# Kernel tuning notes

Measured on AMD Instinct MI355X. Metric: run time of the kernel, lower is better.

Reference implementation:

```python
import jax, jax.numpy as jnp
import numpy as np

N, H, D = 65536, 8, 32      # n_points, num_heads, dim_per_head (h_dim)
CD = 3                      # coords_dim
NW = 3                      # num_w_per_dist
BS = 128                    # block_size
NH = 2                      # n_hashes


def layer_norm(x, g, b, eps=1e-5):
    mu = x.mean(-1, keepdims=True)
    var = ((x - mu) ** 2).mean(-1, keepdims=True)
    return (x - mu) * jax.lax.rsqrt(var + eps) * g + b


def hept_attn(q, k, v, pe, Wrpe):
    """HEPT-style LSH-sorted block-diagonal attention with relative-position kernel.
    q,k,v: (N,H,D); pe: (N,CD); Wrpe: (NW*(CD-1), H*D) (w_rpe.weight^T).
    score_ij = q_i.k_j/sqrt(D) - sum_r omega[h,r]*(p_i,r - p_j,r)^2 within LSH blocks.
    """
    # per-head, per-distance-dim nonnegative RPE weights derived from w_rpe.weight
    omega = (Wrpe.T.reshape(H, D, CD - 1, NW) ** 2).mean(axis=(1, 3))  # (H, CD-1)
    # E2LSH-style random projections of coordinates -> NH scalar hash codes
    proj = jax.random.normal(jax.random.key(42), (NH, CD), dtype=q.dtype)
    codes = pe @ proj.T  # (N, NH)
    scale = 1.0 / jnp.sqrt(jnp.asarray(D, q.dtype))
    nb = N // BS
    out = jnp.zeros((N, H * D), dtype=q.dtype)
    for r in range(NH):
        order = jnp.argsort(codes[:, r])
        inv = jnp.argsort(order)
        qs = q[order].reshape(nb, BS, H, D)
        ks = k[order].reshape(nb, BS, H, D)
        vs = v[order].reshape(nb, BS, H, D)
        ps = pe[order][:, : CD - 1].reshape(nb, BS, CD - 1)
        scores = jnp.einsum("bqhd,bkhd->bhqk", qs, ks) * scale      # (nb,H,BS,BS)
        diff2 = (ps[:, :, None, :] - ps[:, None, :, :]) ** 2        # (nb,BS,BS,CD-1)
        scores = scores - jnp.einsum("hr,bqkr->bhqk", omega, diff2)
        attn = jax.nn.softmax(scores, axis=-1)
        o = jnp.einsum("bhqk,bkhd->bqhd", attn, vs).reshape(N, H * D)
        out = out + o[inv]
    return out / NH


def setup_inputs() -> dict:
    key = jax.random.key(0)
    ks = jax.random.split(key, 16)
    s = 0.02
    return {
        "x": jax.random.normal(ks[0], (N, D), jnp.float32),
        "coords": jax.random.uniform(ks[1], (N, CD), jnp.float32),
        "g1": jnp.ones((D,), jnp.float32),
        "be1": jnp.zeros((D,), jnp.float32),
        "Wq": jax.random.normal(ks[2], (D, H * D), jnp.float32) * s,
        "Wk": jax.random.normal(ks[3], (D, H * D), jnp.float32) * s,
        "Wv": jax.random.normal(ks[4], (D, H * D), jnp.float32) * s,
        "Wrpe": jax.random.normal(ks[5], (NW * (CD - 1), H * D), jnp.float32) * s,
        "Wo": jax.random.normal(ks[6], (H * D, D), jnp.float32) * s,
        "bo": jnp.zeros((D,), jnp.float32),
        "g2": jnp.ones((D,), jnp.float32),
        "be2": jnp.zeros((D,), jnp.float32),
        "W1": jax.random.normal(ks[7], (D, D), jnp.float32) * s,
        "b1": jnp.zeros((D,), jnp.float32),
        "W2": jax.random.normal(ks[8], (D, D), jnp.float32) * s,
        "b2": jnp.zeros((D,), jnp.float32),
    }


def reference(x, coords, g1, be1, Wq, Wk, Wv, Wrpe, Wo, bo, g2, be2, W1, b1, W2, b2):
    # pe_type == 'none' -> pe = coords, x_pe = x (no additive PE)
    xn = layer_norm(x, g1, be1)
    q = (xn @ Wq).reshape(N, H, D)
    k = (xn @ Wk).reshape(N, H, D)
    v = (xn @ Wv).reshape(N, H, D)
    aggr = hept_attn(q, k, v, coords, Wrpe)
    x = x + aggr @ Wo + bo                       # residual (dropout = identity, eval)
    h = layer_norm(x, g2, be2)
    ff = jax.nn.relu(h @ W1 + b1) @ W2 + b2
    return x + ff
```

## Files before the change

kernel.cpp:

```cpp
#include <hip/hip_runtime.h>
#include <stdint.h>

typedef uint32_t u32;
typedef unsigned long long u64;
typedef unsigned short ushort;
typedef __attribute__((ext_vector_type(8))) short short8;
typedef __attribute__((ext_vector_type(4))) float f32x4;

#define NPTS 65536
#define HEADS 8
#define DIM 32
#define HD 256
#define BSZ 128
#define NBLK 512
#define SCALE_QK 0.17677669529663687f
#define LOG2E 1.4426950408889634f

__device__ __forceinline__ u32 rotl32(u32 v, int r){ return (v << r) | (v >> (32 - r)); }

__device__ void threefry2x32_0_42(u32 x0, u32 x1, u32& o0, u32& o1){
  const u32 ks0 = 0u, ks1 = 42u;
  const u32 ks2 = ks0 ^ ks1 ^ 0x1BD11BDAu;
  x0 += ks0; x1 += ks1;
#define TF_RND(r) { x0 += x1; x1 = rotl32(x1, (r)); x1 ^= x0; }
  TF_RND(13) TF_RND(15) TF_RND(26) TF_RND(6)
  x0 += ks1; x1 += ks2 + 1u;
  TF_RND(17) TF_RND(29) TF_RND(16) TF_RND(24)
  x0 += ks2; x1 += ks0 + 2u;
  TF_RND(13) TF_RND(15) TF_RND(26) TF_RND(6)
  x0 += ks0; x1 += ks1 + 3u;
  TF_RND(17) TF_RND(29) TF_RND(16) TF_RND(24)
  x0 += ks1; x1 += ks2 + 4u;
  TF_RND(13) TF_RND(15) TF_RND(26) TF_RND(6)
  x0 += ks2; x1 += ks0 + 5u;
#undef TF_RND
  o0 = x0; o1 = x1;
}

__device__ float erfinv_xla_f32(float x){
  float w = -log1pf(-x * x);
  float p;
  if (w < 5.0f){
    w = w - 2.5f;
    p =            2.81022636e-08f;
    p = fmaf(p, w, 3.43273939e-07f);
    p = fmaf(p, w, -3.5233877e-06f);
    p = fmaf(p, w, -4.39150654e-06f);
    p = fmaf(p, w,  0.00021858087f);
    p = fmaf(p, w, -0.00125372503f);
    p = fmaf(p, w, -0.00417768164f);
    p = fmaf(p, w,  0.246640727f);
    p = fmaf(p, w,  1.50140941f);
  } else {
    w = sqrtf(w) - 3.0f;
    p =            -0.000200214257f;
    p = fmaf(p, w,  0.000100950558f);
    p = fmaf(p, w,  0.00134934322f);
    p = fmaf(p, w, -0.00367342844f);
    p = fmaf(p, w,  0.00573950773f);
    p = fmaf(p, w, -0.0076224613f);
    p = fmaf(p, w,  0.00943887047f);
    p = fmaf(p, w,  1.00167406f);
    p = fmaf(p, w,  2.83297682f);
  }
  return p * x;
}

__device__ float jax_normal_from_bits(u32 bits){
  float f = __uint_as_float((bits >> 9) | 0x3f800000u) - 1.0f;
  const float mn = -0.99999994f;
  float v = fmaf(f, 2.0f, mn);
  v = fmaxf(mn, v);
  return 1.41421356237309505f * erfinv_xla_f32(v);
}

__device__ __forceinline__ ushort f2bf(float f){
  union { __bf16 b; ushort u; } cv;
  cv.b = (__bf16)f;
  return cv.u;
}

__global__ __launch_bounds__(1024) void k_sort2048(const float* __restrict__ coords,
                                                   const float* __restrict__ Wrpe,
                                                   float* __restrict__ omega,
                                                   u64* __restrict__ A0, u64* __restrict__ A1){
  __shared__ u64 sh[2048];
  int t = threadIdx.x;
  int bb = blockIdx.x;
  int r = (bb >= 32);
  u64* A = r ? A1 : A0;
  int base = (bb & 31) * 2048;

  float pr[3];
  #pragma unroll
  for (int j = 0; j < 3; j++){
    u32 a, b;
    threefry2x32_0_42((u32)j, (u32)(j + 3), a, b);
    pr[j] = jax_normal_from_bits(r ? b : a);
  }
  #pragma unroll
  for (int half = 0; half < 2; half++){
    int idx = base + t + half*1024;
    float c0 = coords[idx*3+0], c1 = coords[idx*3+1], c2 = coords[idx*3+2];
    float code = fmaf(c2, pr[2], fmaf(c1, pr[1], c0*pr[0]));
    u32 u = __float_as_uint(code);
    u32 key = (u & 0x80000000u) ? ~u : (u | 0x80000000u);
    sh[t + half*1024] = ((u64)key << 32) | (u64)(u32)idx;
  }
  __syncthreads();
  for (int k = 2; k <= 2048; k <<= 1){
    for (int j = k >> 1; j > 0; j >>= 1){
      int idx = ((t & ~(j-1)) << 1) | (t & (j-1));
      int par = idx | j;
      bool up = ((idx & k) == 0);
      u64 a = sh[idx], b = sh[par];
      if ((a > b) == up){ sh[idx] = b; sh[par] = a; }
      __syncthreads();
    }
  }
  A[base + t] = sh[t];
  A[base + t + 1024] = sh[t + 1024];

  if (bb == 0 && t < 16){
    int h = t >> 1, rr = t & 1;
    float s = 0.f;
    for (int wi = 0; wi < 3; wi++)
      for (int d = 0; d < 32; d++){
        float w = Wrpe[(rr*3 + wi)*HD + h*32 + d];
        s = fmaf(w, w, s);
      }
    omega[t] = s * (1.0f/96.0f);
  }
}

template<int NRG>
__global__ void k_merge2(const u64* __restrict__ s0, const u64* __restrict__ s1,
                         u64* __restrict__ d0, u64* __restrict__ d1, int lgL){
  int gb = blockIdx.x;
  const u64* src = (gb < 256) ? s0 : s1;
  u64*       dst = (gb < 256) ? d0 : d1;
  int g = (gb & 255) * 256 + threadIdx.x;
  int L = 1 << lgL;
  u64 e = src[g];
  int myrun = (g >> lgL) & (NRG - 1);
  int gbase = g & ~(NRG*L - 1);
  int pos = g & (L - 1);
  #pragma unroll
  for (int o = 0; o < NRG; o++){
    if (o == myrun) continue;
    const u64* run = src + gbase + o*L;
    int lo = 0, hi = L;
    while (lo < hi){
      int mid = (lo + hi) >> 1;
      if (run[mid] < e) lo = mid + 1; else hi = mid;
    }
    pos += lo;
  }
  dst[gbase + pos] = e;
}

__global__ __launch_bounds__(256, 4) void k_attn(const u64* __restrict__ s0,
    const u64* __restrict__ s1,
    const float* __restrict__ x, const float* __restrict__ g1, const float* __restrict__ be1,
    const float* __restrict__ coords,
    const float* __restrict__ Wq, const float* __restrict__ Wk, const float* __restrict__ Wv,
    const float* __restrict__ omega, ushort* __restrict__ ag0, ushort* __restrict__ ag1){
  __shared__ __align__(16) char smem[38400];
  ushort* Xs = (ushort*)(smem + 0);
  ushort* Wt = (ushort*)(smem + 10240);
  ushort* Ps = (ushort*)(smem + 0);
  ushort* Ks = (ushort*)(smem + 17920);
  ushort* Vt = (ushort*)(smem + 28160);
  int*    gq_s = (int*)(smem + 36864);
  float2* ps_s = (float2*)(smem + 37376);

  const int bid = blockIdx.x;
  const int h = bid >> 10;
  const int b = (bid >> 1) & 511;
  const int r = bid & 1;
  const u64* sorted = r ? s1 : s0;
  ushort* aggr = r ? ag1 : ag0;

  const int t = threadIdx.x;
  const int w = t >> 6, l = t & 63, lg = l >> 4, lc = l & 15;
  const int R = w * 32;

  if (t < 128){
    int gp = (int)(u32)(sorted[b*BSZ + t] & 0xffffffffull);
    gq_s[t] = gp;
    float2 pc; pc.x = coords[gp*3+0]; pc.y = coords[gp*3+1];
    ps_s[t] = pc;
    float xr[32];
    const float4* xp = (const float4*)(x + (size_t)gp*32);
    #pragma unroll
    for (int c4 = 0; c4 < 8; c4++){
      float4 f = xp[c4];
      xr[c4*4+0]=f.x; xr[c4*4+1]=f.y; xr[c4*4+2]=f.z; xr[c4*4+3]=f.w;
    }
    float mu = 0.f;
    #pragma unroll
    for (int c = 0; c < 32; c++) mu += xr[c];
    mu *= (1.0f/32.0f);
    float var = 0.f;
    #pragma unroll
    for (int c = 0; c < 32; c++){ float d = xr[c]-mu; var = fmaf(d, d, var); }
    var *= (1.0f/32.0f);
    float rs = rsqrtf(var + 1e-5f);
    u32 pk[16];
    #pragma unroll
    for (int i = 0; i < 16; i++){
      float a = (xr[2*i  ]-mu)*rs*g1[2*i  ] + be1[2*i  ];
      float c = (xr[2*i+1]-mu)*rs*g1[2*i+1] + be1[2*i+1];
      pk[i] = (u32)f2bf(a) | ((u32)f2bf(c) << 16);
    }
    #pragma unroll
    for (int q4 = 0; q4 < 4; q4++)
      *(uint4*)&Xs[t*40 + q4*8] = *(uint4*)&pk[q4*4];
  } else {
    int tt = t - 128;
    #pragma unroll
    for (int e = 0; e < 24; e++){
      int flat = tt + e*128;
      int c  = (flat >> 5) & 31;
      int dl = flat & 31;
      const float* Wm = (e < 8) ? Wq : (e < 16) ? Wk : Wv;
      int m = e >> 3;
      float wv_ = Wm[c*HD + h*32 + dl];
      if (e < 8) wv_ *= SCALE_QK * LOG2E;
      Wt[(m*32 + dl)*40 + c] = f2bf(wv_);
    }
  }
  __syncthreads();

  f32x4 qtc[2][2];
  {
    short8 a0 = *(const short8*)&Xs[(R      + lc)*40 + lg*8];
    short8 a1 = *(const short8*)&Xs[(R + 16 + lc)*40 + lg*8];
    short8 wq0 = *(const short8*)&Wt[(     lc)*40 + lg*8];
    short8 wq1 = *(const short8*)&Wt[(16 + lc)*40 + lg*8];
    qtc[0][0] = __builtin_amdgcn_mfma_f32_16x16x32_bf16(wq0, a0, (f32x4){0.f,0.f,0.f,0.f}, 0, 0, 0);
    qtc[0][1] = __builtin_amdgcn_mfma_f32_16x16x32_bf16(wq0, a1, (f32x4){0.f,0.f,0.f,0.f}, 0, 0, 0);
    qtc[1][0] = __builtin_amdgcn_mfma_f32_16x16x32_bf16(wq1, a0, (f32x4){0.f,0.f,0.f,0.f}, 0, 0, 0);
    qtc[1][1] = __builtin_amdgcn_mfma_f32_16x16x32_bf16(wq1, a1, (f32x4){0.f,0.f,0.f,0.f}, 0, 0, 0);
    #pragma unroll
    for (int ct = 2; ct < 6; ct++){
      short8 bb = *(const short8*)&Wt[(ct*16 + lc)*40 + lg*8];
      f32x4 d0 = __builtin_amdgcn_mfma_f32_16x16x32_bf16(a0, bb, (f32x4){0.f,0.f,0.f,0.f}, 0, 0, 0);
      f32x4 d1 = __builtin_amdgcn_mfma_f32_16x16x32_bf16(a1, bb, (f32x4){0.f,0.f,0.f,0.f}, 0, 0, 0);
      #pragma unroll
      for (int i = 0; i < 4; i++){
        int r0 = R + lg*4 + i, r1 = r0 + 16;
        if (ct < 4){
          Ks[r0*40 + (ct-2)*16 + lc] = f2bf(d0[i]);
          Ks[r1*40 + (ct-2)*16 + lc] = f2bf(d1[i]);
        } else {
          Vt[((ct-4)*16 + lc)*136 + r0] = f2bf(d0[i]);
          Vt[((ct-4)*16 + lc)*136 + r1] = f2bf(d1[i]);
        }
      }
    }
  }
  __syncthreads();

  short8 aqv[2];
  #pragma unroll
  for (int qt = 0; qt < 2; qt++){
    u32 wrd[4];
    float prev = 0.f;
    #pragma unroll
    for (int j = 0; j < 8; j++){
      int src = ((lg & 1)*2 + (j >> 2))*16 + lc;
      float t0 = __shfl(qtc[0][qt][j & 3], src, 64);
      float t1 = __shfl(qtc[1][qt][j & 3], src, 64);
      float v = (lg < 2) ? t0 : t1;
      if (j & 1) wrd[j >> 1] = (u32)f2bf(prev) | ((u32)f2bf(v) << 16);
      prev = v;
    }
    aqv[qt] = *(short8*)&wrd[0];
  }

  const float om0 = omega[h*2+0] * LOG2E, om1 = omega[h*2+1] * LOG2E;
  short8 aAug[2];
  #pragma unroll
  for (int qt = 0; qt < 2; qt++){
    float2 pq = ps_s[R + qt*16 + lc];
    u32 wrd[4];
    wrd[0] = (lg == 0) ? ((u32)f2bf(2.0f*om0*pq.x) | ((u32)f2bf(2.0f*om1*pq.y) << 16)) : 0u;
    wrd[1] = (lg == 0) ? (u32)f2bf(1.0f) : 0u;
    wrd[2] = 0u; wrd[3] = 0u;
    aAug[qt] = *(short8*)&wrd[0];
  }

  f32x4 acc[2][8];
  #pragma unroll
  for (int kt = 0; kt < 8; kt++){
    short8 bk = *(const short8*)&Ks[(kt*16 + lc)*40 + lg*8];
    float2 pk = ps_s[kt*16 + lc];
    float nK = -fmaf(om0, pk.x*pk.x, om1*(pk.y*pk.y));
    u32 wrd[4];
    wrd[0] = (lg == 0) ? ((u32)f2bf(pk.x) | ((u32)f2bf(pk.y) << 16)) : 0u;
    wrd[1] = (lg == 0) ? (u32)f2bf(nK) : 0u;
    wrd[2] = 0u; wrd[3] = 0u;
    short8 bAug = *(short8*)&wrd[0];
    acc[0][kt] = __builtin_amdgcn_mfma_f32_16x16x32_bf16(aqv[0], bk, (f32x4){0.f,0.f,0.f,0.f}, 0, 0, 0);
    acc[1][kt] = __builtin_amdgcn_mfma_f32_16x16x32_bf16(aqv[1], bk, (f32x4){0.f,0.f,0.f,0.f}, 0, 0, 0);
    acc[0][kt] = __builtin_amdgcn_mfma_f32_16x16x32_bf16(aAug[0], bAug, acc[0][kt], 0, 0, 0);
    acc[1][kt] = __builtin_amdgcn_mfma_f32_16x16x32_bf16(aAug[1], bAug, acc[1][kt], 0, 0, 0);
  }

  float lrow[2][4] = {{0.f,0.f,0.f,0.f},{0.f,0.f,0.f,0.f}};
  #pragma unroll
  for (int qt = 0; qt < 2; qt++)
    #pragma unroll
    for (int kt = 0; kt < 8; kt++)
      #pragma unroll
      for (int i = 0; i < 4; i++){
        float e = exp2f(acc[qt][kt][i]);
        acc[qt][kt][i] = e;
        lrow[qt][i] += e;
      }
  #pragma unroll
  for (int qt = 0; qt < 2; qt++)
    #pragma unroll
    for (int i = 0; i < 4; i++){
      float s = lrow[qt][i];
      s += __shfl_xor(s, 1);
      s += __shfl_xor(s, 2);
      s += __shfl_xor(s, 4);
      s += __shfl_xor(s, 8);
      lrow[qt][i] = 0.5f / s;
    }

  short8 bv[4][2];
  #pragma unroll
  for (int cc = 0; cc < 4; cc++)
    #pragma unroll
    for (int dt = 0; dt < 2; dt++)
      bv[cc][dt] = *(const short8*)&Vt[(dt*16 + lc)*136 + cc*32 + lg*8];

  ushort* Psw = Ps + w*16*136;
  f32x4 o_acc[2][2];
  #pragma unroll
  for (int qt = 0; qt < 2; qt++)
    #pragma unroll
    for (int dt = 0; dt < 2; dt++) o_acc[qt][dt] = (f32x4){0.f,0.f,0.f,0.f};

  #pragma unroll
  for (int qt = 0; qt < 2; qt++){
    asm volatile("s_waitcnt lgkmcnt(0)" ::: "memory");
    __builtin_amdgcn_sched_barrier(0);
    #pragma unroll
    for (int kt = 0; kt < 8; kt++)
      #pragma unroll
      for (int i = 0; i < 4; i++)
        Psw[(lg*4 + i)*136 + kt*16 + lc] = f2bf(acc[qt][kt][i]);
    asm volatile("s_waitcnt lgkmcnt(0)" ::: "memory");
    __builtin_amdgcn_sched_barrier(0);
    __builtin_amdgcn_s_setprio(1);
    #pragma unroll
    for (int cc = 0; cc < 4; cc++){
      short8 ap = *(const short8*)&Psw[lc*136 + cc*32 + lg*8];
      o_acc[qt][0] = __builtin_amdgcn_mfma_f32_16x16x32_bf16(ap, bv[cc][0], o_acc[qt][0], 0, 0, 0);
      o_acc[qt][1] = __builtin_amdgcn_mfma_f32_16x16x32_bf16(ap, bv[cc][1], o_acc[qt][1], 0, 0, 0);
    }
    __builtin_amdgcn_s_setprio(0);
  }

  #pragma unroll
  for (int qt = 0; qt < 2; qt++)
    #pragma unroll
    for (int i = 0; i < 4; i++){
      int row = R + qt*16 + lg*4 + i;
      int g = gq_s[row];
      ushort* dst = aggr + (size_t)g*HD + h*32 + lc;
      dst[0]  = f2bf(o_acc[qt][0][i] * lrow[qt][i]);
      dst[16] = f2bf(o_acc[qt][1][i] * lrow[qt][i]);
    }
}

__global__ __launch_bounds__(256) void k_out(const float* __restrict__ x,
    const ushort* __restrict__ ag0, const ushort* __restrict__ ag1,
    const float* __restrict__ Wo, const float* __restrict__ bo,
    const float* __restrict__ g2, const float* __restrict__ be2,
    const float* __restrict__ W1, const float* __restrict__ b1,
    const float* __restrict__ W2, const float* __restrict__ b2,
    float* __restrict__ out){
  __shared__ ushort Wot[32*264];
  __shared__ ushort W1t[32*40];
  __shared__ ushort W2t[32*40];
  __shared__ ushort Bnc[4][16*40];
  int t = threadIdx.x;
  #pragma unroll
  for (int e = 0; e < 32; e++){
    int flat = t + e*256;
    int k = flat >> 5, col = flat & 31;
    Wot[col*264 + k] = f2bf(Wo[flat]);
  }
  #pragma unroll
  for (int e = 0; e < 4; e++){
    int flat = t + e*256;
    int k = flat >> 5, col = flat & 31;
    W1t[col*40 + k] = f2bf(W1[flat]);
    W2t[col*40 + k] = f2bf(W2[flat]);
  }
  __syncthreads();

  const int w = t >> 6, l = t & 63, lg = l >> 4, lc = l & 15;
  const int r0 = blockIdx.x*64 + w*16;

  f32x4 acc[2];
  acc[0] = (f32x4){0.f,0.f,0.f,0.f};
  acc[1] = (f32x4){0.f,0.f,0.f,0.f};
  #pragma unroll
  for (int ks = 0; ks < 8; ks++){
    short8 a0 = *(const short8*)(ag0 + (size_t)(r0+lc)*256 + ks*32 + lg*8);
    short8 a1 = *(const short8*)(ag1 + (size_t)(r0+lc)*256 + ks*32 + lg*8);
    #pragma unroll
    for (int ct = 0; ct < 2; ct++){
      short8 bb = *(const short8*)&Wot[(ct*16 + lc)*264 + ks*32 + lg*8];
      acc[ct] = __builtin_amdgcn_mfma_f32_16x16x32_bf16(a0, bb, acc[ct], 0, 0, 0);
      acc[ct] = __builtin_amdgcn_mfma_f32_16x16x32_bf16(a1, bb, acc[ct], 0, 0, 0);
    }
  }
  float x2v[2][4];
  #pragma unroll
  for (int ct = 0; ct < 2; ct++){
    int col = ct*16 + lc;
    float bov = bo[col];
    #pragma unroll
    for (int i = 0; i < 4; i++){
      int row = r0 + lg*4 + i;
      x2v[ct][i] = x[row*32 + col] + acc[ct][i] + bov;
    }
  }

  float g2v[2], be2v[2], b1v[2], b2v[2];
  #pragma unroll
  for (int ct = 0; ct < 2; ct++){
    int col = ct*16 + lc;
    g2v[ct] = g2[col]; be2v[ct] = be2[col]; b1v[ct] = b1[col]; b2v[ct] = b2[col];
  }
  ushort* B = &Bnc[w][0];
  #pragma unroll
  for (int i = 0; i < 4; i++){
    float m = x2v[0][i] + x2v[1][i];
    m += __shfl_xor(m, 1); m += __shfl_xor(m, 2);
    m += __shfl_xor(m, 4); m += __shfl_xor(m, 8);
    float mu = m * (1.0f/32.0f);
    float d0 = x2v[0][i] - mu, d1 = x2v[1][i] - mu;
    float v = fmaf(d0, d0, d1*d1);
    v += __shfl_xor(v, 1); v += __shfl_xor(v, 2);
    v += __shfl_xor(v, 4); v += __shfl_xor(v, 8);
    float rs = rsqrtf(v * (1.0f/32.0f) + 1e-5f);
    B[(lg*4 + i)*40 +      lc] = f2bf(d0 * rs * g2v[0] + be2v[0]);
    B[(lg*4 + i)*40 + 16 + lc] = f2bf(d1 * rs * g2v[1] + be2v[1]);
  }
  asm volatile("s_waitcnt lgkmcnt(0)" ::: "memory");
  __builtin_amdgcn_sched_barrier(0);

  short8 ha = *(const short8*)&B[lc*40 + lg*8];
  f32x4 f1[2];
  #pragma unroll
  for (int ct = 0; ct < 2; ct++){
    short8 bb = *(const short8*)&W1t[(ct*16 + lc)*40 + lg*8];
    f1[ct] = __builtin_amdgcn_mfma_f32_16x16x32_bf16(ha, bb, (f32x4){0.f,0.f,0.f,0.f}, 0, 0, 0);
  }
  asm volatile("s_waitcnt lgkmcnt(0)" ::: "memory");
  __builtin_amdgcn_sched_barrier(0);
  #pragma unroll
  for (int ct = 0; ct < 2; ct++)
    #pragma unroll
    for (int i = 0; i < 4; i++)
      B[(lg*4 + i)*40 + ct*16 + lc] = f2bf(fmaxf(f1[ct][i] + b1v[ct], 0.f));
  asm volatile("s_waitcnt lgkmcnt(0)" ::: "memory");
  __builtin_amdgcn_sched_barrier(0);

  short8 ta = *(const short8*)&B[lc*40 + lg*8];
  #pragma unroll
  for (int ct = 0; ct < 2; ct++){
    short8 bb = *(const short8*)&W2t[(ct*16 + lc)*40 + lg*8];
    f32x4 f2 = __builtin_amdgcn_mfma_f32_16x16x32_bf16(ta, bb, (f32x4){0.f,0.f,0.f,0.f}, 0, 0, 0);
    int col = ct*16 + lc;
    #pragma unroll
    for (int i = 0; i < 4; i++){
      int row = r0 + lg*4 + i;
      out[row*32 + col] = x2v[ct][i] + f2[i] + b2v[ct];
    }
  }
}

extern "C" void kernel_launch(void* const* d_in, const int* in_sizes, int n_in,
                              void* d_out, int out_size, void* d_ws, size_t ws_size,
                              hipStream_t stream) {
  (void)in_sizes; (void)n_in; (void)out_size; (void)ws_size;
  const float* x      = (const float*)d_in[0];
  const float* coords = (const float*)d_in[1];
  const float* g1     = (const float*)d_in[2];
  const float* be1    = (const float*)d_in[3];
  const float* Wq     = (const float*)d_in[4];
  const float* Wk     = (const float*)d_in[5];
  const float* Wv     = (const float*)d_in[6];
  const float* Wrpe   = (const float*)d_in[7];
  const float* Wo     = (const float*)d_in[8];
  const float* bo     = (const float*)d_in[9];
  const float* g2     = (const float*)d_in[10];
  const float* be2    = (const float*)d_in[11];
  const float* W1     = (const float*)d_in[12];
  const float* b1     = (const float*)d_in[13];
  const float* W2     = (const float*)d_in[14];
  const float* b2     = (const float*)d_in[15];
  float* out = (float*)d_out;

  char* ws = (char*)d_ws;
  ushort* ag0   = (ushort*)(ws + 0);
  ushort* ag1   = (ushort*)(ws + 33554432);
  u64*   keyA0  = (u64*)  (ws + 67108864);
  u64*   keyA1  = (u64*)  (ws + 67633152);
  u64*   keyB0  = (u64*)  (ws + 68157440);
  u64*   keyB1  = (u64*)  (ws + 68681728);
  float* omega  = (float*)(ws + 69206016);

  k_sort2048<<<64, 1024, 0, stream>>>(coords, Wrpe, omega, keyA0, keyA1);
  k_merge2<4><<<512, 256, 0, stream>>>(keyA0, keyA1, keyB0, keyB1, 11);
  k_merge2<4><<<512, 256, 0, stream>>>(keyB0, keyB1, keyA0, keyA1, 13);
  k_merge2<2><<<512, 256, 0, stream>>>(keyA0, keyA1, keyB0, keyB1, 15);

  k_attn<<<NBLK*HEADS*2, 256, 0, stream>>>(keyB0, keyB1, x, g1, be1, coords,
                                           Wq, Wk, Wv, omega, ag0, ag1);

  k_out<<<NPTS/64, 256, 0, stream>>>(x, ag0, ag1, Wo, bo, g2, be2, W1, b1, W2, b2, out);
}
```

Measured before the change: 158.1 us.

## Precompute LayerNorm once in sort kernel and gather bf16 rows in attention

The first LayerNorm moves into the sort kernel. It is computed once per point and written to a bf16 buffer, so the attention kernel no longer recomputes it for each of 16 (head, hash) blocks. k_attn gathers the normalized rows directly from global memory into MFMA operands, which removes the Xs shared tile. Shared memory drops from 38400 to 28160 bytes and launch bounds rise to 5 blocks per CU to raise occupancy. An extra __syncthreads is added, presumably because Ps now aliases the Wt/Ks region. The cost is an extra global buffer write and read, plus scattered 16-byte global gathers on the MFMA critical path.

```diff
diff --git a/kernel.cpp b/kernel.cpp
--- a/kernel.cpp
+++ b/kernel.cpp
@@ -82,7 +82,11 @@
 
 __global__ __launch_bounds__(1024) void k_sort2048(const float* __restrict__ coords,
                                                    const float* __restrict__ Wrpe,
+                                                   const float* __restrict__ x,
+                                                   const float* __restrict__ g1,
+                                                   const float* __restrict__ be1,
                                                    float* __restrict__ omega,
+                                                   ushort* __restrict__ xn,
                                                    u64* __restrict__ A0, u64* __restrict__ A1){
   __shared__ u64 sh[2048];
   int t = threadIdx.x;
@@ -90,6 +94,30 @@
   int r = (bb >= 32);
   u64* A = r ? A1 : A0;
   int base = (bb & 31) * 2048;
+
+  {
+    int gt = bb*1024 + t;
+    const float4* xp = (const float4*)(x + (size_t)gt*32);
+    float mu = 0.f, s2 = 0.f;
+    #pragma unroll
+    for (int c4 = 0; c4 < 8; c4++){
+      float4 f = xp[c4];
+      mu += f.x + f.y + f.z + f.w;
+      s2 = fmaf(f.x,f.x, fmaf(f.y,f.y, fmaf(f.z,f.z, fmaf(f.w,f.w, s2))));
+    }
+    mu *= (1.0f/32.0f);
+    float var = fmaf(-mu, mu, s2*(1.0f/32.0f));
+    float rs = rsqrtf(var + 1e-5f);
+    #pragma unroll
+    for (int c4 = 0; c4 < 8; c4++){
+      float4 f = xp[c4];
+      u32 w0 = (u32)f2bf((f.x-mu)*rs*g1[c4*4+0] + be1[c4*4+0])
+             | ((u32)f2bf((f.y-mu)*rs*g1[c4*4+1] + be1[c4*4+1]) << 16);
+      u32 w1 = (u32)f2bf((f.z-mu)*rs*g1[c4*4+2] + be1[c4*4+2])
+             | ((u32)f2bf((f.w-mu)*rs*g1[c4*4+3] + be1[c4*4+3]) << 16);
+      *(uint2*)&xn[(size_t)gt*32 + c4*4] = make_uint2(w0, w1);
+    }
+  }
 
   float pr[3];
   #pragma unroll
@@ -159,20 +187,18 @@
   dst[gbase + pos] = e;
 }
 
-__global__ __launch_bounds__(256, 4) void k_attn(const u64* __restrict__ s0,
+__global__ __launch_bounds__(256, 5) void k_attn(const u64* __restrict__ s0,
     const u64* __restrict__ s1,
-    const float* __restrict__ x, const float* __restrict__ g1, const float* __restrict__ be1,
-    const float* __restrict__ coords,
+    const ushort* __restrict__ xn, const float* __restrict__ coords,
     const float* __restrict__ Wq, const float* __restrict__ Wk, const float* __restrict__ Wv,
     const float* __restrict__ omega, ushort* __restrict__ ag0, ushort* __restrict__ ag1){
-  __shared__ __align__(16) char smem[38400];
-  ushort* Xs = (ushort*)(smem + 0);
-  ushort* Wt = (ushort*)(smem + 10240);
+  __shared__ __align__(16) char smem[28160];
+  ushort* Wt = (ushort*)(smem + 0);
+  ushort* Ks = (ushort*)(smem + 7680);
   ushort* Ps = (ushort*)(smem + 0);
-  ushort* Ks = (ushort*)(smem + 17920);
-  ushort* Vt = (ushort*)(smem + 28160);
-  int*    gq_s = (int*)(smem + 36864);
-  float2* ps_s = (float2*)(smem + 37376);
+  ushort* Vt = (ushort*)(smem + 17920);
+  int*    gq_s = (int*)(smem + 26624);
+  float2* ps_s = (float2*)(smem + 27136);
 
   const int bid = blockIdx.x;
   const int h = bid >> 10;
@@ -185,57 +211,29 @@
   const int w = t >> 6, l = t & 63, lg = l >> 4, lc = l & 15;
   const int R = w * 32;
 
+  #pragma unroll
+  for (int e = 0; e < 12; e++){
+    int flat = t + e*256;
+    int m   = flat >> 10;
+    int rem = flat & 1023;
+    int c   = rem >> 5, dl = rem & 31;
+    const float* Wm = (m == 0) ? Wq : (m == 1) ? Wk : Wv;
+    float wv_ = Wm[c*HD + h*32 + dl];
+    if (m == 0) wv_ *= SCALE_QK * LOG2E;
+    Wt[(m*32 + dl)*40 + c] = f2bf(wv_);
+  }
   if (t < 128){
     int gp = (int)(u32)(sorted[b*BSZ + t] & 0xffffffffull);
     gq_s[t] = gp;
     float2 pc; pc.x = coords[gp*3+0]; pc.y = coords[gp*3+1];
     ps_s[t] = pc;
-    float xr[32];
-    const float4* xp = (const float4*)(x + (size_t)gp*32);
-    #pragma unroll
-    for (int c4 = 0; c4 < 8; c4++){
-      float4 f = xp[c4];
-      xr[c4*4+0]=f.x; xr[c4*4+1]=f.y; xr[c4*4+2]=f.z; xr[c4*4+3]=f.w;
-    }
-    float mu = 0.f;
-    #pragma unroll
-    for (int c = 0; c < 32; c++) mu += xr[c];
-    mu *= (1.0f/32.0f);
-    float var = 0.f;
-    #pragma unroll
-    for (int c = 0; c < 32; c++){ float d = xr[c]-mu; var = fmaf(d, d, var); }
-    var *= (1.0f/32.0f);
-    float rs = rsqrtf(var + 1e-5f);
-    u32 pk[16];
-    #pragma unroll
-    for (int i = 0; i < 16; i++){
-      float a = (xr[2*i  ]-mu)*rs*g1[2*i  ] + be1[2*i  ];
-      float c = (xr[2*i+1]-mu)*rs*g1[2*i+1] + be1[2*i+1];
-      pk[i] = (u32)f2bf(a) | ((u32)f2bf(c) << 16);
-    }
-    #pragma unroll
-    for (int q4 = 0; q4 < 4; q4++)
-      *(uint4*)&Xs[t*40 + q4*8] = *(uint4*)&pk[q4*4];
-  } else {
-    int tt = t - 128;
-    #pragma unroll
-    for (int e = 0; e < 24; e++){
-      int flat = tt + e*128;
-      int c  = (flat >> 5) & 31;
-      int dl = flat & 31;
-      const float* Wm = (e < 8) ? Wq : (e < 16) ? Wk : Wv;
-      int m = e >> 3;
-      float wv_ = Wm[c*HD + h*32 + dl];
-      if (e < 8) wv_ *= SCALE_QK * LOG2E;
-      Wt[(m*32 + dl)*40 + c] = f2bf(wv_);
-    }
   }
   __syncthreads();
 
   f32x4 qtc[2][2];
   {
-    short8 a0 = *(const short8*)&Xs[(R      + lc)*40 + lg*8];
-    short8 a1 = *(const short8*)&Xs[(R + 16 + lc)*40 + lg*8];
+    short8 a0 = *(const short8*)(xn + (size_t)gq_s[R      + lc]*32 + lg*8);
+    short8 a1 = *(const short8*)(xn + (size_t)gq_s[R + 16 + lc]*32 + lg*8);
     short8 wq0 = *(const short8*)&Wt[(     lc)*40 + lg*8];
     short8 wq1 = *(const short8*)&Wt[(16 + lc)*40 + lg*8];
     qtc[0][0] = __builtin_amdgcn_mfma_f32_16x16x32_bf16(wq0, a0, (f32x4){0.f,0.f,0.f,0.f}, 0, 0, 0);
@@ -307,6 +305,7 @@
     acc[0][kt] = __builtin_amdgcn_mfma_f32_16x16x32_bf16(aAug[0], bAug, acc[0][kt], 0, 0, 0);
     acc[1][kt] = __builtin_amdgcn_mfma_f32_16x16x32_bf16(aAug[1], bAug, acc[1][kt], 0, 0, 0);
   }
+  __syncthreads();
 
   float lrow[2][4] = {{0.f,0.f,0.f,0.f},{0.f,0.f,0.f,0.f}};
   #pragma unroll
@@ -514,18 +513,19 @@
   char* ws = (char*)d_ws;
   ushort* ag0   = (ushort*)(ws + 0);
   ushort* ag1   = (ushort*)(ws + 33554432);
-  u64*   keyA0  = (u64*)  (ws + 67108864);
-  u64*   keyA1  = (u64*)  (ws + 67633152);
-  u64*   keyB0  = (u64*)  (ws + 68157440);
-  u64*   keyB1  = (u64*)  (ws + 68681728);
-  float* omega  = (float*)(ws + 69206016);
-
-  k_sort2048<<<64, 1024, 0, stream>>>(coords, Wrpe, omega, keyA0, keyA1);
+  ushort* xn    = (ushort*)(ws + 67108864);
+  u64*   keyA0  = (u64*)  (ws + 71303168);
+  u64*   keyA1  = (u64*)  (ws + 71827456);
+  u64*   keyB0  = (u64*)  (ws + 72351744);
+  u64*   keyB1  = (u64*)  (ws + 72876032);
+  float* omega  = (float*)(ws + 73400320);
+
+  k_sort2048<<<64, 1024, 0, stream>>>(coords, Wrpe, x, g1, be1, omega, xn, keyA0, keyA1);
   k_merge2<4><<<512, 256, 0, stream>>>(keyA0, keyA1, keyB0, keyB1, 11);
   k_merge2<4><<<512, 256, 0, stream>>>(keyB0, keyB1, keyA0, keyA1, 13);
   k_merge2<2><<<512, 256, 0, stream>>>(keyA0, keyA1, keyB0, keyB1, 15);
 
-  k_attn<<<NBLK*HEADS*2, 256, 0, stream>>>(keyB0, keyB1, x, g1, be1, coords,
+  k_attn<<<NBLK*HEADS*2, 256, 0, stream>>>(keyB0, keyB1, xn, coords,
                                            Wq, Wk, Wv, omega, ag0, ag1);
 
   k_out<<<NPTS/64, 256, 0, stream>>>(x, ag0, ag1, Wo, bo, g2, be2, W1, b1, W2, b2, out);
```

After: 184.2 us. 1.17x slower.
